# Optimization experiments

Hardware: AMD Instinct MI355X
Metric: run time of the kernel (lower is better)

Reference implementation:

```python
import math
import jax, jax.numpy as jnp
import numpy as np

H = 16  # n_heads


def setup_inputs() -> dict:
    key = jax.random.key(0)
    ks = jax.random.split(key, 12)
    b, n, dm = 4, 1024, 1024
    s = 1.0 / math.sqrt(dm)
    inp = {
        'query': jax.random.normal(ks[0], (b, n, dm), jnp.float32),
        'key':   jax.random.normal(ks[1], (b, n, dm), jnp.float32),
        'value': jax.random.normal(ks[2], (b, n, dm), jnp.float32),
        'Wq': jax.random.normal(ks[3], (dm, dm), jnp.float32) * s,
        'bq': jnp.zeros((dm,), jnp.float32),
        'Wk': jax.random.normal(ks[4], (dm, dm), jnp.float32) * s,
        'bk': jnp.zeros((dm,), jnp.float32),
        'Wv': jax.random.normal(ks[5], (dm, dm), jnp.float32) * s,
        'bv': jnp.zeros((dm,), jnp.float32),
        'Wo': jax.random.normal(ks[6], (dm, dm), jnp.float32) * s,
        'bo': jnp.zeros((dm,), jnp.float32),
    }
    return inp


def reference(query, key, value, Wq, bq, Wk, bk, Wv, bv, Wo, bo):
    b, n, dm = query.shape
    dk = dm // H

    def proj(x, W, bias):
        # Linear(d_model,d_model) then split heads: [b,n,dm] -> [b,h,n,dk]
        y = x @ W.T + bias
        return y.reshape(b, n, H, dk).transpose(0, 2, 1, 3)

    q = proj(query, Wq, bq)
    k = proj(key, Wk, bk)
    v = proj(value, Wv, bv)

    scores = jnp.einsum('bhid,bhjd->bhij', q, k) / math.sqrt(dk)  # [b,h,n,n]
    p_attn = jax.nn.softmax(scores, axis=-1)
    # softmax(ones) along last dim is exactly uniform 1/n
    p_ident = jnp.full_like(scores, 1.0 / n)
    rnd = jax.random.normal(jax.random.key(42), scores.shape, scores.dtype)
    p_rand = jax.nn.softmax(rnd, axis=-1)

    # FAITHFUL to source: einsum('b h i j, b h i d -> b h i d', p, value)
    # i.e. value scaled by row-sum of the attention probs (== value up to numerics)
    def weight(p):
        return v * jnp.sum(p, axis=-1, keepdims=True)  # [b,h,n,dk]

    x = weight(p_attn)
    y = weight(p_ident)
    z = weight(p_rand)

    def merge(t):  # [b,h,n,dk] -> [b,n,dm]
        return t.transpose(0, 2, 1, 3).reshape(b, n, dm)

    return (merge(x) @ Wo.T + bo, merge(y), merge(z))
```

## Files before the change

### kernel.cpp

```cpp
#include <hip/hip_runtime.h>
#include <hip/hip_bf16.h>
#include <stdint.h>

using bf16 = __hip_bfloat16;
typedef __attribute__((ext_vector_type(8))) __bf16 bf16x8;
typedef __attribute__((ext_vector_type(4))) float f32x4;

static __device__ __forceinline__ bf16 f2b(float x) { return __float2bfloat16(x); }

__global__ __launch_bounds__(256) void prep_kernel(
    const float* __restrict__ value, const float* __restrict__ Wv,
    const float* __restrict__ Wo, const float* __restrict__ bv,
    const float* __restrict__ bo,
    bf16* __restrict__ value_b, bf16* __restrict__ Wv_b,
    bf16* __restrict__ Wo_b, bf16* __restrict__ WvT_b,
    float* __restrict__ bc,
    int nbVal, int nbW, int nbT, int dm)
{
    const int b = blockIdx.x;
    const int tid = threadIdx.x;

    if (b < nbVal) {
        const size_t i = ((size_t)b * 256 + tid) * 4;
        const float4 v = *(const float4*)(value + i);
        bf16 h0 = f2b(v.x), h1 = f2b(v.y), h2 = f2b(v.z), h3 = f2b(v.w);
        uint2 u;
        u.x = (uint32_t)(*(const uint16_t*)&h0) | ((uint32_t)(*(const uint16_t*)&h1) << 16);
        u.y = (uint32_t)(*(const uint16_t*)&h2) | ((uint32_t)(*(const uint16_t*)&h3) << 16);
        *(uint2*)(value_b + i) = u;
    } else if (b < nbVal + nbW) {
        const size_t i = ((size_t)(b - nbVal) * 256 + tid) * 4;
        const float4 v = *(const float4*)(Wo + i);
        bf16 h0 = f2b(v.x), h1 = f2b(v.y), h2 = f2b(v.z), h3 = f2b(v.w);
        uint2 u;
        u.x = (uint32_t)(*(const uint16_t*)&h0) | ((uint32_t)(*(const uint16_t*)&h1) << 16);
        u.y = (uint32_t)(*(const uint16_t*)&h2) | ((uint32_t)(*(const uint16_t*)&h3) << 16);
        *(uint2*)(Wo_b + i) = u;
    } else if (b < nbVal + nbW + nbT) {
        __shared__ bf16 tile[32][33];
        const int t = b - nbVal - nbW;
        const int tpr = dm / 32;
        const int i0 = (t / tpr) * 32, j0 = (t % tpr) * 32;
        const int tx = tid & 31, ty = tid >> 5;
        #pragma unroll
        for (int p = 0; p < 4; ++p) {
            const int r = ty + p * 8;
            const float v = Wv[(size_t)(i0 + r) * dm + j0 + tx];
            const bf16 h = f2b(v);
            Wv_b[(size_t)(i0 + r) * dm + j0 + tx] = h;
            tile[r][tx] = h;
        }
        __syncthreads();
        #pragma unroll
        for (int p = 0; p < 4; ++p) {
            const int c = ty + p * 8;
            WvT_b[(size_t)(j0 + c) * dm + i0 + tx] = tile[tx][c];
        }
    } else {
        __shared__ float red[4];
        const int row = b - nbVal - nbW - nbT;
        const float* wrow = Wo + (size_t)row * dm;
        float s = 0.f;
        for (int k = tid; k < dm; k += 256) s += wrow[k] * bv[k];
        #pragma unroll
        for (int off = 32; off >= 1; off >>= 1) s += __shfl_down(s, off, 64);
        if ((tid & 63) == 0) red[tid >> 6] = s;
        __syncthreads();
        if (tid == 0) bc[row] = red[0] + red[1] + red[2] + red[3] + bo[row];
    }
}

__global__ __launch_bounds__(256) void gemm64_bt_b16out(
    const bf16* __restrict__ A, const bf16* __restrict__ B,
    bf16* __restrict__ C, int M, int N, int K)
{
    __shared__ bf16 As[64 * 32];
    __shared__ bf16 Bs[64 * 32];

    const int tid = threadIdx.x;
    const int lane = tid & 63;
    const int wave = tid >> 6;
    const int wm = (wave >> 1) * 32;
    const int wn = (wave & 1) * 32;
    const int bm = blockIdx.x * 64;
    const int bn = blockIdx.y * 64;

    f32x4 acc[2][2] = {};

    const int c = wave * 64 + lane;
    const bf16* gA = A + (size_t)(bm + (c >> 2)) * K + (c & 3) * 8;
    const bf16* gB = B + (size_t)(bn + (c >> 2)) * K + (c & 3) * 8;
    bf16* lA = As + (size_t)c * 8;
    bf16* lB = Bs + (size_t)c * 8;

    const int fr = lane & 15;
    const int fk = (lane >> 4) * 8;

    for (int k0 = 0; k0 < K; k0 += 32) {
        __builtin_amdgcn_global_load_lds(
            (const __attribute__((address_space(1))) void*)(gA + k0),
            (__attribute__((address_space(3))) void*)lA, 16, 0, 0);
        __builtin_amdgcn_global_load_lds(
            (const __attribute__((address_space(1))) void*)(gB + k0),
            (__attribute__((address_space(3))) void*)lB, 16, 0, 0);
        __syncthreads();
        bf16x8 af[2], bg[2];
        #pragma unroll
        for (int t = 0; t < 2; ++t) {
            af[t] = *(const bf16x8*)(As + (wm + t * 16 + fr) * 32 + fk);
            bg[t] = *(const bf16x8*)(Bs + (wn + t * 16 + fr) * 32 + fk);
        }
        #pragma unroll
        for (int i = 0; i < 2; ++i)
            #pragma unroll
            for (int j = 0; j < 2; ++j)
                acc[i][j] = __builtin_amdgcn_mfma_f32_16x16x32_bf16(
                    af[i], bg[j], acc[i][j], 0, 0, 0);
        __syncthreads();
    }

    const int quad = lane >> 4;
    #pragma unroll
    for (int j = 0; j < 2; ++j) {
        const int col = bn + wn + j * 16 + fr;
        #pragma unroll
        for (int i = 0; i < 2; ++i) {
            const int row0 = bm + wm + i * 16 + quad * 4;
            #pragma unroll
            for (int r = 0; r < 4; ++r)
                C[(size_t)(row0 + r) * N + col] = f2b(acc[i][j][r]);
        }
    }
}

#define TM 128
#define TN 128
#define BK 32

__global__ __launch_bounds__(256) void gemm_fused(
    const bf16* __restrict__ A, const bf16* __restrict__ Bcat,
    const float* __restrict__ bv, const float* __restrict__ bc,
    float* __restrict__ out0, float* __restrict__ out1, float* __restrict__ out2,
    int M, int dm)
{
    __shared__ bf16 As[TM * BK];
    __shared__ bf16 Bs[TN * BK];

    const int K = dm;
    const int tid = threadIdx.x;
    const int lane = tid & 63;
    const int wave = tid >> 6;
    const int wm = (wave >> 1) * 64;
    const int wn = (wave & 1) * 64;
    const int bm = blockIdx.x * TM;
    const int bn = blockIdx.y * TN;

    f32x4 acc[4][4] = {};

    const int c0 = wave * 128 + lane;
    const int c1 = c0 + 64;
    const bf16* gA0 = A + (size_t)(bm + (c0 >> 2)) * K + (c0 & 3) * 8;
    const bf16* gA1 = A + (size_t)(bm + (c1 >> 2)) * K + (c1 & 3) * 8;
    const bf16* gB0 = Bcat + (size_t)(bn + (c0 >> 2)) * K + (c0 & 3) * 8;
    const bf16* gB1 = Bcat + (size_t)(bn + (c1 >> 2)) * K + (c1 & 3) * 8;
    bf16* lA0 = As + (size_t)(wave * 128) * 8;
    bf16* lA1 = lA0 + 64 * 8;
    bf16* lB0 = Bs + (size_t)(wave * 128) * 8;
    bf16* lB1 = lB0 + 64 * 8;

    const int fr = lane & 15;
    const int fk = (lane >> 4) * 8;

    for (int k0 = 0; k0 < K; k0 += BK) {
        __builtin_amdgcn_global_load_lds(
            (const __attribute__((address_space(1))) void*)(gA0 + k0),
            (__attribute__((address_space(3))) void*)lA0, 16, 0, 0);
        __builtin_amdgcn_global_load_lds(
            (const __attribute__((address_space(1))) void*)(gA1 + k0),
            (__attribute__((address_space(3))) void*)lA1, 16, 0, 0);
        __builtin_amdgcn_global_load_lds(
            (const __attribute__((address_space(1))) void*)(gB0 + k0),
            (__attribute__((address_space(3))) void*)lB0, 16, 0, 0);
        __builtin_amdgcn_global_load_lds(
            (const __attribute__((address_space(1))) void*)(gB1 + k0),
            (__attribute__((address_space(3))) void*)lB1, 16, 0, 0);
        __syncthreads();

        bf16x8 af[4], bg[4];
        #pragma unroll
        for (int t = 0; t < 4; ++t) {
            af[t] = *(const bf16x8*)(As + (wm + t * 16 + fr) * BK + fk);
            bg[t] = *(const bf16x8*)(Bs + (wn + t * 16 + fr) * BK + fk);
        }
        #pragma unroll
        for (int i = 0; i < 4; ++i)
            #pragma unroll
            for (int j = 0; j < 4; ++j)
                acc[i][j] = __builtin_amdgcn_mfma_f32_16x16x32_bf16(
                    af[i], bg[j], acc[i][j], 0, 0, 0);
        __syncthreads();
    }

    const bool second = (bn >= dm);
    const int cb = bn + wn - (second ? dm : 0);
    const float* bias = second ? bc : bv;
    float* o0 = second ? out0 : out1;
    float* o1 = second ? nullptr : out2;
    const int quad = lane >> 4;
    #pragma unroll
    for (int j = 0; j < 4; ++j) {
        const int col = cb + j * 16 + fr;
        const float bb = bias[col];
        #pragma unroll
        for (int i = 0; i < 4; ++i) {
            const int row0 = bm + wm + i * 16 + quad * 4;
            #pragma unroll
            for (int r = 0; r < 4; ++r) {
                const float v = acc[i][j][r] + bb;
                const size_t idx = (size_t)(row0 + r) * dm + col;
                o0[idx] = v;
                if (o1) o1[idx] = v;
            }
        }
    }
}

__global__ __launch_bounds__(256) void gemm_f32_naive(
    const float* __restrict__ A, const float* __restrict__ B,
    const float* __restrict__ bias,
    float* __restrict__ C0, float* __restrict__ C1,
    int M, int N, int K)
{
    const size_t idx = (size_t)blockIdx.x * 256 + threadIdx.x;
    if (idx >= (size_t)M * N) return;
    const int row = (int)(idx / N), col = (int)(idx % N);
    const float* a = A + (size_t)row * K;
    const float* b = B + (size_t)col * K;
    float s = bias ? bias[col] : 0.0f;
    for (int k = 0; k < K; ++k) s += a[k] * b[k];
    C0[idx] = s;
    if (C1) C1[idx] = s;
}

extern "C" void kernel_launch(void* const* d_in, const int* in_sizes, int n_in,
                              void* d_out, int out_size, void* d_ws, size_t ws_size,
                              hipStream_t stream)
{
    const float* value = (const float*)d_in[2];
    const float* Wv    = (const float*)d_in[7];
    const float* bv    = (const float*)d_in[8];
    const float* Wo    = (const float*)d_in[9];
    const float* bo    = (const float*)d_in[10];

    const int dm = in_sizes[8];
    const int M  = in_sizes[2] / dm;
    const size_t MN = (size_t)M * dm;

    float* out0 = (float*)d_out;
    float* out1 = out0 + MN;
    float* out2 = out1 + MN;

    const size_t need = MN * 2 + (size_t)dm * dm * 2 * 4 + (size_t)dm * 4;
    const bool ok = (ws_size >= need) && (M % TM == 0) && (dm % TM == 0) &&
                    (dm % 32 == 0) && (MN % 1024 == 0);
    if (ok) {
        char* ws = (char*)d_ws;
        bf16* value_b = (bf16*)ws;                                   ws += MN * 2;
        bf16* Wv_b    = (bf16*)ws;                                   ws += (size_t)dm * dm * 2;
        bf16* Wc_b    = (bf16*)ws;                                   ws += (size_t)dm * dm * 2;
        bf16* Wo_b    = (bf16*)ws;                                   ws += (size_t)dm * dm * 2;
        bf16* WvT_b   = (bf16*)ws;                                   ws += (size_t)dm * dm * 2;
        float* bc     = (float*)ws;

        const int nbVal = (int)(MN / 1024);
        const int nbW   = dm * dm / 1024;
        const int nbT   = (dm / 32) * (dm / 32);
        prep_kernel<<<nbVal + nbW + nbT + dm, 256, 0, stream>>>(
            value, Wv, Wo, bv, bo, value_b, Wv_b, Wo_b, WvT_b, bc,
            nbVal, nbW, nbT, dm);

        dim3 g64(dm / 64, dm / 64);
        gemm64_bt_b16out<<<g64, 256, 0, stream>>>(Wo_b, WvT_b, Wc_b, dm, dm, dm);

        dim3 grid(M / TM, 2 * dm / TN);
        gemm_fused<<<grid, 256, 0, stream>>>(value_b, Wv_b ,
                                             bv, bc, out0, out1, out2, M, dm);
    } else {
        const int nblk = (int)((MN + 255) / 256);
        gemm_f32_naive<<<nblk, 256, 0, stream>>>(value, Wv, bv, out1, out2, M, dm, dm);
        gemm_f32_naive<<<nblk, 256, 0, stream>>>(out1, Wo, bo, out0, nullptr, M, dm, dm);
    }
}
```

Measured before the change: 165.2 us.

## Fuse Wo·Wv combine GEMM into prep kernel, swizzle LDS, vectorize epilogue stores

Merges the separate combined-weight GEMM into the prep kernel, which now converts Wo and Wv from fp32 on the fly and transposes Wv inside shared memory. This removes one launch and the Wo_b/WvT_b intermediate buffers. The main GEMM gets an XOR swizzle on its LDS tile to cut bank conflicts. Its epilogue is staged through shared memory so each row is written with float4 stores instead of scalar ones. The bias-combine path is also vectorized to one wave per row. The risk is that the folded GEMM blocks run slower than the dedicated kernel and become a tail in the prep launch.

```diff
diff --git a/kernel.cpp b/kernel.cpp
--- a/kernel.cpp
+++ b/kernel.cpp
@@ -7,128 +7,110 @@
 typedef __attribute__((ext_vector_type(4))) float f32x4;
 
 static __device__ __forceinline__ bf16 f2b(float x) { return __float2bfloat16(x); }
-
-__global__ __launch_bounds__(256) void prep_kernel(
+static __device__ __forceinline__ uint32_t pack2(float a, float b) {
+    bf16 ha = f2b(a), hb = f2b(b);
+    return (uint32_t)(*(const uint16_t*)&ha) | ((uint32_t)(*(const uint16_t*)&hb) << 16);
+}
+
+__global__ __launch_bounds__(256) void prep_wc_kernel(
     const float* __restrict__ value, const float* __restrict__ Wv,
     const float* __restrict__ Wo, const float* __restrict__ bv,
     const float* __restrict__ bo,
     bf16* __restrict__ value_b, bf16* __restrict__ Wv_b,
-    bf16* __restrict__ Wo_b, bf16* __restrict__ WvT_b,
-    float* __restrict__ bc,
-    int nbVal, int nbW, int nbT, int dm)
-{
+    bf16* __restrict__ Wc_b, float* __restrict__ bc,
+    int nbVal, int nbWv, int nbBc, int dm)
+{
+    __shared__ bf16 dAs[64 * 40];
+    __shared__ bf16 dBs[64 * 40];
+
     const int b = blockIdx.x;
     const int tid = threadIdx.x;
 
     if (b < nbVal) {
-        const size_t i = ((size_t)b * 256 + tid) * 4;
-        const float4 v = *(const float4*)(value + i);
-        bf16 h0 = f2b(v.x), h1 = f2b(v.y), h2 = f2b(v.z), h3 = f2b(v.w);
-        uint2 u;
-        u.x = (uint32_t)(*(const uint16_t*)&h0) | ((uint32_t)(*(const uint16_t*)&h1) << 16);
-        u.y = (uint32_t)(*(const uint16_t*)&h2) | ((uint32_t)(*(const uint16_t*)&h3) << 16);
-        *(uint2*)(value_b + i) = u;
-    } else if (b < nbVal + nbW) {
-        const size_t i = ((size_t)(b - nbVal) * 256 + tid) * 4;
-        const float4 v = *(const float4*)(Wo + i);
-        bf16 h0 = f2b(v.x), h1 = f2b(v.y), h2 = f2b(v.z), h3 = f2b(v.w);
-        uint2 u;
-        u.x = (uint32_t)(*(const uint16_t*)&h0) | ((uint32_t)(*(const uint16_t*)&h1) << 16);
-        u.y = (uint32_t)(*(const uint16_t*)&h2) | ((uint32_t)(*(const uint16_t*)&h3) << 16);
-        *(uint2*)(Wo_b + i) = u;
-    } else if (b < nbVal + nbW + nbT) {
-        __shared__ bf16 tile[32][33];
-        const int t = b - nbVal - nbW;
-        const int tpr = dm / 32;
-        const int i0 = (t / tpr) * 32, j0 = (t % tpr) * 32;
-        const int tx = tid & 31, ty = tid >> 5;
-        #pragma unroll
-        for (int p = 0; p < 4; ++p) {
-            const int r = ty + p * 8;
-            const float v = Wv[(size_t)(i0 + r) * dm + j0 + tx];
-            const bf16 h = f2b(v);
-            Wv_b[(size_t)(i0 + r) * dm + j0 + tx] = h;
-            tile[r][tx] = h;
-        }
-        __syncthreads();
-        #pragma unroll
-        for (int p = 0; p < 4; ++p) {
-            const int c = ty + p * 8;
-            WvT_b[(size_t)(j0 + c) * dm + i0 + tx] = tile[tx][c];
-        }
-    } else {
-        __shared__ float red[4];
-        const int row = b - nbVal - nbW - nbT;
+        const size_t i = ((size_t)b * 256 + tid) * 8;
+        const float4 v0 = *(const float4*)(value + i);
+        const float4 v1 = *(const float4*)(value + i + 4);
+        uint4 u = { pack2(v0.x, v0.y), pack2(v0.z, v0.w),
+                    pack2(v1.x, v1.y), pack2(v1.z, v1.w) };
+        *(uint4*)(value_b + i) = u;
+    } else if (b < nbVal + nbWv) {
+        const size_t i = ((size_t)(b - nbVal) * 256 + tid) * 8;
+        const float4 v0 = *(const float4*)(Wv + i);
+        const float4 v1 = *(const float4*)(Wv + i + 4);
+        uint4 u = { pack2(v0.x, v0.y), pack2(v0.z, v0.w),
+                    pack2(v1.x, v1.y), pack2(v1.z, v1.w) };
+        *(uint4*)(Wv_b + i) = u;
+    } else if (b < nbVal + nbWv + nbBc) {
+        const int lane = tid & 63;
+        const int wave = tid >> 6;
+        const int row = (b - nbVal - nbWv) * 4 + wave;
         const float* wrow = Wo + (size_t)row * dm;
         float s = 0.f;
-        for (int k = tid; k < dm; k += 256) s += wrow[k] * bv[k];
+        for (int k = lane * 4; k < dm; k += 256) {
+            const float4 w = *(const float4*)(wrow + k);
+            const float4 x = *(const float4*)(bv + k);
+            s += w.x * x.x + w.y * x.y + w.z * x.z + w.w * x.w;
+        }
         #pragma unroll
         for (int off = 32; off >= 1; off >>= 1) s += __shfl_down(s, off, 64);
-        if ((tid & 63) == 0) red[tid >> 6] = s;
-        __syncthreads();
-        if (tid == 0) bc[row] = red[0] + red[1] + red[2] + red[3] + bo[row];
-    }
-}
-
-__global__ __launch_bounds__(256) void gemm64_bt_b16out(
-    const bf16* __restrict__ A, const bf16* __restrict__ B,
-    bf16* __restrict__ C, int M, int N, int K)
-{
-    __shared__ bf16 As[64 * 32];
-    __shared__ bf16 Bs[64 * 32];
-
-    const int tid = threadIdx.x;
-    const int lane = tid & 63;
-    const int wave = tid >> 6;
-    const int wm = (wave >> 1) * 32;
-    const int wn = (wave & 1) * 32;
-    const int bm = blockIdx.x * 64;
-    const int bn = blockIdx.y * 64;
-
-    f32x4 acc[2][2] = {};
-
-    const int c = wave * 64 + lane;
-    const bf16* gA = A + (size_t)(bm + (c >> 2)) * K + (c & 3) * 8;
-    const bf16* gB = B + (size_t)(bn + (c >> 2)) * K + (c & 3) * 8;
-    bf16* lA = As + (size_t)c * 8;
-    bf16* lB = Bs + (size_t)c * 8;
-
-    const int fr = lane & 15;
-    const int fk = (lane >> 4) * 8;
-
-    for (int k0 = 0; k0 < K; k0 += 32) {
-        __builtin_amdgcn_global_load_lds(
-            (const __attribute__((address_space(1))) void*)(gA + k0),
-            (__attribute__((address_space(3))) void*)lA, 16, 0, 0);
-        __builtin_amdgcn_global_load_lds(
-            (const __attribute__((address_space(1))) void*)(gB + k0),
-            (__attribute__((address_space(3))) void*)lB, 16, 0, 0);
-        __syncthreads();
-        bf16x8 af[2], bg[2];
-        #pragma unroll
-        for (int t = 0; t < 2; ++t) {
-            af[t] = *(const bf16x8*)(As + (wm + t * 16 + fr) * 32 + fk);
-            bg[t] = *(const bf16x8*)(Bs + (wn + t * 16 + fr) * 32 + fk);
-        }
-        #pragma unroll
-        for (int i = 0; i < 2; ++i)
-            #pragma unroll
-            for (int j = 0; j < 2; ++j)
-                acc[i][j] = __builtin_amdgcn_mfma_f32_16x16x32_bf16(
-                    af[i], bg[j], acc[i][j], 0, 0, 0);
-        __syncthreads();
-    }
-
-    const int quad = lane >> 4;
-    #pragma unroll
-    for (int j = 0; j < 2; ++j) {
-        const int col = bn + wn + j * 16 + fr;
-        #pragma unroll
-        for (int i = 0; i < 2; ++i) {
-            const int row0 = bm + wm + i * 16 + quad * 4;
-            #pragma unroll
-            for (int r = 0; r < 4; ++r)
-                C[(size_t)(row0 + r) * N + col] = f2b(acc[i][j][r]);
+        if (lane == 0) bc[row] = s + bo[row];
+    } else {
+        const int t = b - nbVal - nbWv - nbBc;
+        const int tpr = dm / 64;
+        const int bm = (t / tpr) * 64, bn = (t % tpr) * 64;
+        const int lane = tid & 63;
+        const int wave = tid >> 6;
+        const int wm = (wave >> 1) * 32, wn = (wave & 1) * 32;
+        const int fr = lane & 15;
+        const int fkc = lane >> 4;
+
+        f32x4 acc[2][2] = {};
+
+        for (int k0 = 0; k0 < dm; k0 += 32) {
+            {
+                const int r = tid >> 2, col = (tid & 3) * 8;
+                const float4 v0 = *(const float4*)(Wo + (size_t)(bm + r) * dm + k0 + col);
+                const float4 v1 = *(const float4*)(Wo + (size_t)(bm + r) * dm + k0 + col + 4);
+                uint4 u = { pack2(v0.x, v0.y), pack2(v0.z, v0.w),
+                            pack2(v1.x, v1.y), pack2(v1.z, v1.w) };
+                *(uint4*)(dAs + r * 40 + col) = u;
+            }
+            #pragma unroll
+            for (int q = 0; q < 2; ++q) {
+                const int fidx = tid + q * 256;
+                const int kk = fidx >> 4, c4 = (fidx & 15) * 4;
+                const float4 v = *(const float4*)(Wv + (size_t)(k0 + kk) * dm + bn + c4);
+                dBs[(c4 + 0) * 40 + kk] = f2b(v.x);
+                dBs[(c4 + 1) * 40 + kk] = f2b(v.y);
+                dBs[(c4 + 2) * 40 + kk] = f2b(v.z);
+                dBs[(c4 + 3) * 40 + kk] = f2b(v.w);
+            }
+            __syncthreads();
+            bf16x8 af[2], bg[2];
+            #pragma unroll
+            for (int u = 0; u < 2; ++u) {
+                af[u] = *(const bf16x8*)(dAs + (wm + u * 16 + fr) * 40 + fkc * 8);
+                bg[u] = *(const bf16x8*)(dBs + (wn + u * 16 + fr) * 40 + fkc * 8);
+            }
+            #pragma unroll
+            for (int i = 0; i < 2; ++i)
+                #pragma unroll
+                for (int j = 0; j < 2; ++j)
+                    acc[i][j] = __builtin_amdgcn_mfma_f32_16x16x32_bf16(
+                        af[i], bg[j], acc[i][j], 0, 0, 0);
+            __syncthreads();
+        }
+        const int quad = lane >> 4;
+        #pragma unroll
+        for (int j = 0; j < 2; ++j) {
+            const int col = bn + wn + j * 16 + fr;
+            #pragma unroll
+            for (int i = 0; i < 2; ++i) {
+                const int row0 = bm + wm + i * 16 + quad * 4;
+                #pragma unroll
+                for (int r = 0; r < 4; ++r)
+                    Wc_b[(size_t)(row0 + r) * dm + col] = f2b(acc[i][j][r]);
+            }
         }
     }
 }
@@ -145,6 +127,7 @@
 {
     __shared__ bf16 As[TM * BK];
     __shared__ bf16 Bs[TN * BK];
+    __shared__ float Es[4][16 * 68];
 
     const int K = dm;
     const int tid = threadIdx.x;
@@ -157,19 +140,23 @@
 
     f32x4 acc[4][4] = {};
 
-    const int c0 = wave * 128 + lane;
-    const int c1 = c0 + 64;
-    const bf16* gA0 = A + (size_t)(bm + (c0 >> 2)) * K + (c0 & 3) * 8;
-    const bf16* gA1 = A + (size_t)(bm + (c1 >> 2)) * K + (c1 & 3) * 8;
-    const bf16* gB0 = Bcat + (size_t)(bn + (c0 >> 2)) * K + (c0 & 3) * 8;
-    const bf16* gB1 = Bcat + (size_t)(bn + (c1 >> 2)) * K + (c1 & 3) * 8;
-    bf16* lA0 = As + (size_t)(wave * 128) * 8;
-    bf16* lA1 = lA0 + 64 * 8;
-    bf16* lB0 = Bs + (size_t)(wave * 128) * 8;
-    bf16* lB1 = lB0 + 64 * 8;
+    const int s0 = wave * 128 + lane;
+    const int s1 = s0 + 64;
+    const int r0 = s0 >> 2, r1 = s1 >> 2;
+    const int p0 = (s0 & 3) ^ (r0 & 3) ^ ((r0 >> 2) & 3);
+    const int p1 = (s1 & 3) ^ (r1 & 3) ^ ((r1 >> 2) & 3);
+    const bf16* gA0 = A + (size_t)(bm + r0) * K + p0 * 8;
+    const bf16* gA1 = A + (size_t)(bm + r1) * K + p1 * 8;
+    const bf16* gB0 = Bcat + (size_t)(bn + r0) * K + p0 * 8;
+    const bf16* gB1 = Bcat + (size_t)(bn + r1) * K + p1 * 8;
+    bf16* lA0 = As + s0 * 8;
+    bf16* lA1 = As + s1 * 8;
+    bf16* lB0 = Bs + s0 * 8;
+    bf16* lB1 = Bs + s1 * 8;
 
     const int fr = lane & 15;
-    const int fk = (lane >> 4) * 8;
+    const int fkc = lane >> 4;
+    const int xsw = fkc ^ (fr & 3) ^ ((fr >> 2) & 3);
 
     for (int k0 = 0; k0 < K; k0 += BK) {
         __builtin_amdgcn_global_load_lds(
@@ -189,8 +176,8 @@
         bf16x8 af[4], bg[4];
         #pragma unroll
         for (int t = 0; t < 4; ++t) {
-            af[t] = *(const bf16x8*)(As + (wm + t * 16 + fr) * BK + fk);
-            bg[t] = *(const bf16x8*)(Bs + (wn + t * 16 + fr) * BK + fk);
+            af[t] = *(const bf16x8*)(As + (wm + t * 16 + fr) * BK + xsw * 8);
+            bg[t] = *(const bf16x8*)(Bs + (wn + t * 16 + fr) * BK + xsw * 8);
         }
         #pragma unroll
         for (int i = 0; i < 4; ++i)
@@ -202,25 +189,34 @@
     }
 
     const bool second = (bn >= dm);
-    const int cb = bn + wn - (second ? dm : 0);
+    const int colbase = bn + wn - (second ? dm : 0);
     const float* bias = second ? bc : bv;
     float* o0 = second ? out0 : out1;
     float* o1 = second ? nullptr : out2;
+
+    float bb[4];
+    #pragma unroll
+    for (int j = 0; j < 4; ++j) bb[j] = bias[colbase + j * 16 + fr];
+
+    float* E = &Es[wave][0];
     const int quad = lane >> 4;
+    const int rgrp = lane >> 4;
+    const int cc = (lane & 15) * 4;
+
     #pragma unroll
-    for (int j = 0; j < 4; ++j) {
-        const int col = cb + j * 16 + fr;
-        const float bb = bias[col];
-        #pragma unroll
-        for (int i = 0; i < 4; ++i) {
-            const int row0 = bm + wm + i * 16 + quad * 4;
-            #pragma unroll
-            for (int r = 0; r < 4; ++r) {
-                const float v = acc[i][j][r] + bb;
-                const size_t idx = (size_t)(row0 + r) * dm + col;
-                o0[idx] = v;
-                if (o1) o1[idx] = v;
-            }
+    for (int i = 0; i < 4; ++i) {
+        #pragma unroll
+        for (int j = 0; j < 4; ++j)
+            #pragma unroll
+            for (int r = 0; r < 4; ++r)
+                E[(quad * 4 + r) * 68 + j * 16 + fr] = acc[i][j][r] + bb[j];
+        #pragma unroll
+        for (int ph = 0; ph < 4; ++ph) {
+            const int row = rgrp * 4 + ph;
+            const float4 v = *(const float4*)(E + row * 68 + cc);
+            const size_t gi = (size_t)(bm + wm + i * 16 + row) * dm + colbase + cc;
+            *(float4*)(o0 + gi) = v;
+            if (o1) *(float4*)(o1 + gi) = v;
         }
     }
 }
@@ -260,27 +256,24 @@
     float* out1 = out0 + MN;
     float* out2 = out1 + MN;
 
-    const size_t need = MN * 2 + (size_t)dm * dm * 2 * 4 + (size_t)dm * 4;
+    const size_t need = MN * 2 + (size_t)dm * dm * 2 * 2 + (size_t)dm * 4;
     const bool ok = (ws_size >= need) && (M % TM == 0) && (dm % TM == 0) &&
-                    (dm % 32 == 0) && (MN % 1024 == 0);
+                    (MN % 2048 == 0) && ((size_t)dm * dm % 2048 == 0) &&
+                    (dm % 64 == 0) && (dm % 4 == 0);
     if (ok) {
         char* ws = (char*)d_ws;
-        bf16* value_b = (bf16*)ws;                                   ws += MN * 2;
-        bf16* Wv_b    = (bf16*)ws;                                   ws += (size_t)dm * dm * 2;
-        bf16* Wc_b    = (bf16*)ws;                                   ws += (size_t)dm * dm * 2;
-        bf16* Wo_b    = (bf16*)ws;                                   ws += (size_t)dm * dm * 2;
-        bf16* WvT_b   = (bf16*)ws;                                   ws += (size_t)dm * dm * 2;
+        bf16* value_b = (bf16*)ws;                    ws += MN * 2;
+        bf16* Wv_b    = (bf16*)ws;                    ws += (size_t)dm * dm * 2;
+        bf16* Wc_b    = (bf16*)ws;                    ws += (size_t)dm * dm * 2;
         float* bc     = (float*)ws;
 
-        const int nbVal = (int)(MN / 1024);
-        const int nbW   = dm * dm / 1024;
-        const int nbT   = (dm / 32) * (dm / 32);
-        prep_kernel<<<nbVal + nbW + nbT + dm, 256, 0, stream>>>(
-            value, Wv, Wo, bv, bo, value_b, Wv_b, Wo_b, WvT_b, bc,
-            nbVal, nbW, nbT, dm);
-
-        dim3 g64(dm / 64, dm / 64);
-        gemm64_bt_b16out<<<g64, 256, 0, stream>>>(Wo_b, WvT_b, Wc_b, dm, dm, dm);
+        const int nbVal = (int)(MN / 2048);
+        const int nbWv  = (int)((size_t)dm * dm / 2048);
+        const int nbBc  = dm / 4;
+        const int nbWc  = (dm / 64) * (dm / 64);
+        prep_wc_kernel<<<nbVal + nbWv + nbBc + nbWc, 256, 0, stream>>>(
+            value, Wv, Wo, bv, bo, value_b, Wv_b, Wc_b, bc,
+            nbVal, nbWv, nbBc, dm);
 
         dim3 grid(M / TM, 2 * dm / TN);
         gemm_fused<<<grid, 256, 0, stream>>>(value_b, Wv_b ,
```

Result: slower. 190.9 us (+15.6%).
